# Performance work log

Measured on AMD Instinct MI355X. Metric: run time of the kernel, lower is better.

## Reference

```python
import jax, jax.numpy as jnp
import numpy as np

RADIUS = 3
T_STEPS = 2
NEG = -9.0e8
B, L, DEG = 256, 64, 6
FEAT, BOND, FP, OUT = 39, 10, 256, 1


def _leaky(x):
    return jax.nn.leaky_relu(x, 0.01)


def _gru(x, h, wih, whh, bih, bhh):
    # PyTorch GRUCell: gates ordered (r, z, n)
    gi = x @ wih.T + bih
    gh = h @ whh.T + bhh
    ir, iz, inn = jnp.split(gi, 3, axis=-1)
    hr, hz, hn = jnp.split(gh, 3, axis=-1)
    r = jax.nn.sigmoid(ir + hr)
    z = jax.nn.sigmoid(iz + hz)
    n = jnp.tanh(inn + r * hn)
    return (1.0 - z) * n + z * h


def _forward(atom_list, bond_list, atom_mask,
             atom_fc_w, atom_fc_b, neighbor_fc_w, neighbor_fc_b,
             align_w, align_b, attend_w, attend_b,
             gru_wih, gru_whh, gru_bih, gru_bhh,
             mol_align_w, mol_align_b, mol_attend_w, mol_attend_b,
             mol_gru_wih, mol_gru_whh, mol_gru_bih, mol_gru_bhh,
             out_w, out_b,
             atom_degree_list, bond_degree_list):
    b, l, _ = atom_list.shape
    mask = atom_mask[..., None]                                   # [B,L,1]
    atom_feature = _leaky(atom_list @ atom_fc_w.T + atom_fc_b)    # [B,L,FP]

    # per-molecule neighbor gather (padding index = L-1)
    bidx = jnp.arange(b)[:, None, None]
    atom_nb = atom_list[bidx, atom_degree_list]                    # [B,L,deg,FEAT]
    bond_nb = bond_list[bidx, bond_degree_list]                    # [B,L,deg,BOND]
    neighbor_feature = _leaky(
        jnp.concatenate([atom_nb, bond_nb], axis=-1) @ neighbor_fc_w.T + neighbor_fc_b
    )                                                              # [B,L,deg,FP]

    attend_mask = (atom_degree_list != l - 1).astype(atom_feature.dtype)[..., None]
    softmax_mask = jnp.where(atom_degree_list == l - 1, NEG, 0.0).astype(atom_feature.dtype)[..., None]

    for d in range(RADIUS):
        af_exp = jnp.broadcast_to(atom_feature[:, :, None, :], neighbor_feature.shape)
        feature_align = jnp.concatenate([af_exp, neighbor_feature], axis=-1)  # [B,L,deg,2FP]
        align_score = _leaky(feature_align @ align_w[d].T + align_b[d]) + softmax_mask
        attention_weight = jax.nn.softmax(align_score, axis=-2) * attend_mask
        attended = neighbor_feature @ attend_w[d].T + attend_b[d]
        context = jax.nn.elu(jnp.sum(attention_weight * attended, axis=-2))   # [B,L,FP]
        atom_feature = _gru(context.reshape(b * l, -1), atom_feature.reshape(b * l, -1),
                            gru_wih[d], gru_whh[d], gru_bih[d], gru_bhh[d]).reshape(b, l, -1)
        # faithful to original: self-feature broadcast across neighbor dim
        neighbor_feature = jnp.broadcast_to(jax.nn.relu(atom_feature)[:, :, None, :],
                                            neighbor_feature.shape)

    mol_feature = jnp.sum(jax.nn.relu(atom_feature) * mask, axis=-2)          # [B,FP]
    mol_softmax_mask = jnp.where(atom_mask == 0, NEG, 0.0).astype(atom_feature.dtype)[..., None]

    for _ in range(T_STEPS):
        m_exp = jnp.broadcast_to(mol_feature[:, None, :], atom_feature.shape)
        mol_align = jnp.concatenate([m_exp, atom_feature], axis=-1)           # [B,L,2FP]
        mol_score = _leaky(mol_align @ mol_align_w.T + mol_align_b) + mol_softmax_mask
        mol_w = jax.nn.softmax(mol_score, axis=-2) * mask
        attended = atom_feature @ mol_attend_w.T + mol_attend_b
        mol_context = jax.nn.elu(jnp.sum(mol_w * attended, axis=-2))
        mol_feature = _gru(mol_context, mol_feature,
                           mol_gru_wih, mol_gru_whh, mol_gru_bih, mol_gru_bhh)

    mol_prediction = mol_feature @ out_w.T + out_b
    return atom_feature, mol_prediction


def setup_inputs() -> dict:
    key = jax.random.key(0)
    ks = jax.random.split(key, 20)
    s = 0.05
    return {
        "atom_list": jax.random.normal(ks[0], (B, L, FEAT), jnp.float32),
        "bond_list": jax.random.normal(ks[1], (B, L, BOND), jnp.float32),
        "atom_degree_list": jax.random.randint(ks[2], (B, L, DEG), 0, L),
        "bond_degree_list": jax.random.randint(ks[3], (B, L, DEG), 0, L),
        "atom_mask": jnp.ones((B, L), jnp.float32),
        "atom_fc_w": jax.random.normal(ks[4], (FP, FEAT)) * s,
        "atom_fc_b": jnp.zeros((FP,)),
        "neighbor_fc_w": jax.random.normal(ks[5], (FP, FEAT + BOND)) * s,
        "neighbor_fc_b": jnp.zeros((FP,)),
        "align_w": jax.random.normal(ks[6], (RADIUS, 1, 2 * FP)) * s,
        "align_b": jnp.zeros((RADIUS, 1)),
        "attend_w": jax.random.normal(ks[7], (RADIUS, FP, FP)) * s,
        "attend_b": jnp.zeros((RADIUS, FP)),
        "gru_wih": jax.random.normal(ks[8], (RADIUS, 3 * FP, FP)) * s,
        "gru_whh": jax.random.normal(ks[9], (RADIUS, 3 * FP, FP)) * s,
        "gru_bih": jnp.zeros((RADIUS, 3 * FP)),
        "gru_bhh": jnp.zeros((RADIUS, 3 * FP)),
        "mol_align_w": jax.random.normal(ks[10], (1, 2 * FP)) * s,
        "mol_align_b": jnp.zeros((1,)),
        "mol_attend_w": jax.random.normal(ks[11], (FP, FP)) * s,
        "mol_attend_b": jnp.zeros((FP,)),
        "mol_gru_wih": jax.random.normal(ks[12], (3 * FP, FP)) * s,
        "mol_gru_whh": jax.random.normal(ks[13], (3 * FP, FP)) * s,
        "mol_gru_bih": jnp.zeros((3 * FP,)),
        "mol_gru_bhh": jnp.zeros((3 * FP,)),
        "out_w": jax.random.normal(ks[14], (OUT, FP)) * s,
        "out_b": jnp.zeros((OUT,)),
    }


def reference(atom_list, bond_list, atom_degree_list, bond_degree_list, atom_mask,
              atom_fc_w, atom_fc_b, neighbor_fc_w, neighbor_fc_b,
              align_w, align_b, attend_w, attend_b,
              gru_wih, gru_whh, gru_bih, gru_bhh,
              mol_align_w, mol_align_b, mol_attend_w, mol_attend_b,
              mol_gru_wih, mol_gru_whh, mol_gru_bih, mol_gru_bhh,
              out_w, out_b):
    return _forward(atom_list, bond_list, atom_mask,
                    atom_fc_w, atom_fc_b, neighbor_fc_w, neighbor_fc_b,
                    align_w, align_b, attend_w, attend_b,
                    gru_wih, gru_whh, gru_bih, gru_bhh,
                    mol_align_w, mol_align_b, mol_attend_w, mol_attend_b,
                    mol_gru_wih, mol_gru_whh, mol_gru_bih, mol_gru_bhh,
                    out_w, out_b,
                    atom_degree_list, bond_degree_list)
```

## Files before the change

kernel.cpp:

```cpp
#include <hip/hip_runtime.h>
#include <hip/hip_bf16.h>

#define NB 256
#define NL 64
#define DEG 6
#define FEAT 39
#define BOND 10
#define FP 256
#define NEGV (-9.0e8f)

using s16x8 = __attribute__((ext_vector_type(8))) short;
using f32x4 = __attribute__((ext_vector_type(4))) float;

__device__ __forceinline__ unsigned short f2bf(float f){
  unsigned u = __float_as_uint(f);
  u += 0x7fffu + ((u >> 16) & 1u);
  return (unsigned short)(u >> 16);
}
__device__ __forceinline__ float lo16(unsigned u){ return __uint_as_float(u << 16); }
__device__ __forceinline__ float hi16(unsigned u){ return __uint_as_float(u & 0xffff0000u); }

__device__ __forceinline__ float block_sum256(float v, float* scr){
  #pragma unroll
  for(int o=32;o>0;o>>=1) v += __shfl_down(v, o, 64);
  __syncthreads();
  if((threadIdx.x & 63) == 0) scr[threadIdx.x >> 6] = v;
  __syncthreads();
  return scr[0] + scr[1] + scr[2] + scr[3];
}
__device__ __forceinline__ float wave_allsum(float v){
  #pragma unroll
  for(int o=1;o<64;o<<=1) v += __shfl_xor(v, o, 64);
  return v;
}

#define CVT_N0 196608
#define CVT_N1 589824
#define CVT_N2 589824
#define CVT_N3 65536
#define CVT_N4 196608
#define CVT_N5 196608
#define CVT_TOT (CVT_N0+CVT_N1+CVT_N2+CVT_N3+CVT_N4+CVT_N5)

__global__ void k_cvt_all(const float* __restrict__ a0, const float* __restrict__ a1,
                          const float* __restrict__ a2, const float* __restrict__ a3,
                          const float* __restrict__ a4, const float* __restrict__ a5,
                          unsigned short* __restrict__ dst){
  int i = blockIdx.x*256 + threadIdx.x;
  int off = i; const float* src;
  if(off < CVT_N0) src = a0;
  else { off -= CVT_N0;
    if(off < CVT_N1) src = a1;
    else { off -= CVT_N1;
      if(off < CVT_N2) src = a2;
      else { off -= CVT_N2;
        if(off < CVT_N3) src = a3;
        else { off -= CVT_N3;
          if(off < CVT_N4) src = a4;
          else { off -= CVT_N4; src = a5; } } } } }
  dst[i] = f2bf(src[off]);
}

__global__ void k_tr(const float* __restrict__ aw, const float* __restrict__ nw,
                     float* __restrict__ afcT, unsigned short* __restrict__ nfcT){
  int i = blockIdx.x*256 + threadIdx.x;
  if(i < 40*256){
    int k = i >> 8, r = i & 255;
    afcT[i] = (k < FEAT) ? aw[r*FEAT + k] : 0.f;
  } else {
    int j = i - 40*256;
    int k = j >> 8, r = j & 255;
    nfcT[j] = (k < FEAT+BOND) ? f2bf(nw[r*(FEAT+BOND) + k]) : (unsigned short)0;
  }
}

__global__ __launch_bounds__(256) void k_atom4(const float* __restrict__ atom,
    const float* __restrict__ afcT, const float* __restrict__ bias, float* __restrict__ af){
  __shared__ float WT[40*256];
  __shared__ float x_s[4][40];
  const int t = threadIdx.x, bl0 = blockIdx.x*4;
  for(int v=t; v<2560; v+=256) *(float4*)&WT[v*4] = *(const float4*)&afcT[v*4];
  for(int idx=t; idx<4*FEAT; idx+=256){ int a=idx/FEAT, k=idx%FEAT; x_s[a][k]=atom[(bl0+a)*FEAT+k]; }
  if(t < 4) x_s[t][39] = 0.f;
  __syncthreads();
  const int w = t>>6, t0 = (t&63)*4, row = bl0 + w;
  float4 b4 = *(const float4*)&bias[t0];
  float acc[4] = {b4.x, b4.y, b4.z, b4.w};
  for(int k=0;k<40;++k){
    float iv = x_s[w][k];
    float4 wv = *(const float4*)&WT[(k<<8)+t0];
    acc[0]=fmaf(iv,wv.x,acc[0]); acc[1]=fmaf(iv,wv.y,acc[1]);
    acc[2]=fmaf(iv,wv.z,acc[2]); acc[3]=fmaf(iv,wv.w,acc[3]);
  }
  float4 o;
  o.x = acc[0]>0.f?acc[0]:0.01f*acc[0]; o.y = acc[1]>0.f?acc[1]:0.01f*acc[1];
  o.z = acc[2]>0.f?acc[2]:0.01f*acc[2]; o.w = acc[3]>0.f?acc[3]:0.01f*acc[3];
  *(float4*)&af[(size_t)row*FP + t0] = o;
}

__global__ __launch_bounds__(256) void k_nbr4(const float* __restrict__ atom,
    const float* __restrict__ bond, const int* __restrict__ adl, const int* __restrict__ bdl,
    const unsigned short* __restrict__ nfcT, const float* __restrict__ bn,
    const float* __restrict__ alw, const float* __restrict__ alb,
    const float* __restrict__ af, float* __restrict__ wnf, float* __restrict__ swb){
  __shared__ unsigned short WnT[52*256];
  __shared__ float in_s[4][DEG][52];
  __shared__ int   ai_s[4][DEG];
  const int t = threadIdx.x, bl0 = blockIdx.x*4;
  if(t < 24){ int a=t/6, d=t%6; ai_s[a][d] = adl[(bl0+a)*DEG + d]; }
  for(int v=t; v<1664; v+=256) *(s16x8*)&WnT[v*8] = *(const s16x8*)&nfcT[v*8];
  __syncthreads();
  for(int idx=t; idx<4*DEG*(FEAT+BOND); idx+=256){
    int a = idx/(DEG*(FEAT+BOND)), rem = idx%(DEG*(FEAT+BOND));
    int d = rem/(FEAT+BOND), k = rem%(FEAT+BOND);
    int bb = (bl0+a) >> 6;
    float v;
    if(k < FEAT) v = atom[((size_t)bb*NL + ai_s[a][d])*FEAT + k];
    else { int bi = bdl[(bl0+a)*DEG + d]; v = bond[((size_t)bb*NL + bi)*BOND + (k-FEAT)]; }
    in_s[a][d][k] = v;
  }
  if(t < 24){ int a=t/6, d=t%6; in_s[a][d][49]=0.f; in_s[a][d][50]=0.f; in_s[a][d][51]=0.f; }
  __syncthreads();
  const int w = t>>6, lane = t&63, t0 = lane*4, row = bl0 + w;
  float acc[DEG][4] = {};
  for(int k=0;k<52;++k){
    uint2 u = *(const uint2*)&WnT[(k<<8) + t0];
    float w0=lo16(u.x), w1=hi16(u.x), w2=lo16(u.y), w3=hi16(u.y);
    #pragma unroll
    for(int d=0;d<DEG;++d){
      float iv = in_s[w][d][k];
      acc[d][0]=fmaf(iv,w0,acc[d][0]); acc[d][1]=fmaf(iv,w1,acc[d][1]);
      acc[d][2]=fmaf(iv,w2,acc[d][2]); acc[d][3]=fmaf(iv,w3,acc[d][3]);
    }
  }
  float4 bnv = *(const float4*)&bn[t0];
  float bna[4] = {bnv.x, bnv.y, bnv.z, bnv.w};
  float nf[DEG][4];
  #pragma unroll
  for(int d=0;d<DEG;++d)
    #pragma unroll
    for(int j=0;j<4;++j){ float v = acc[d][j] + bna[j]; nf[d][j] = v>0.f ? v : 0.01f*v; }
  float4 af4 = *(const float4*)&af[(size_t)row*FP + t0];
  float4 a1  = *(const float4*)&alw[t0];
  float4 a2  = *(const float4*)&alw[FP + t0];
  float sa = wave_allsum(af4.x*a1.x + af4.y*a1.y + af4.z*a1.z + af4.w*a1.w);
  float sd[DEG];
  #pragma unroll
  for(int d=0;d<DEG;++d)
    sd[d] = wave_allsum(nf[d][0]*a2.x + nf[d][1]*a2.y + nf[d][2]*a2.z + nf[d][3]*a2.w);
  float ab = alb[0];
  float sc[DEG], msk[DEG];
  #pragma unroll
  for(int d=0;d<DEG;++d){
    float v = sa + sd[d] + ab;
    v = v>0.f ? v : 0.01f*v;
    msk[d] = (ai_s[w][d] == NL-1) ? 0.f : 1.f;
    sc[d] = v + (msk[d] > 0.f ? 0.f : NEGV);
  }
  float m = sc[0];
  #pragma unroll
  for(int d=1;d<DEG;++d) m = fmaxf(m, sc[d]);
  float e[DEG], Z = 0.f;
  #pragma unroll
  for(int d=0;d<DEG;++d){ e[d] = expf(sc[d]-m); Z += e[d]; }
  float wgt[DEG], sw = 0.f;
  #pragma unroll
  for(int d=0;d<DEG;++d){ wgt[d] = e[d]/Z*msk[d]; sw += wgt[d]; }
  float o[4] = {};
  #pragma unroll
  for(int d=0;d<DEG;++d)
    #pragma unroll
    for(int j=0;j<4;++j) o[j] = fmaf(wgt[d], nf[d][j], o[j]);
  float4 ov; ov.x=o[0]; ov.y=o[1]; ov.z=o[2]; ov.w=o[3];
  *(float4*)&wnf[(size_t)row*FP + t0] = ov;
  if(lane == 0) swb[row] = sw;
}

template<int MODE>
__global__ __launch_bounds__(256) void k_ctx_gemm(
    const float* __restrict__ Xsrc, const float* __restrict__ swb,
    const unsigned short* __restrict__ Wbf, const float* __restrict__ bat,
    unsigned short* __restrict__ ctxbf){
  __shared__ unsigned short A_lds[64][264];
  __shared__ unsigned short B_lds[64][264];
  const int t = threadIdx.x;
  const int m0 = (blockIdx.x >> 2) * 64, n0 = (blockIdx.x & 3) * 64;
  const int rb = t >> 4, cb = (t & 15) * 16;
  for(int i=0;i<4;++i){
    int row = i*16 + rb;
    const float* src = Xsrc + (size_t)(m0+row)*FP + cb;
    float mult = MODE ? swb[m0+row] : 1.f;
    unsigned short tmp[16];
    #pragma unroll
    for(int q=0;q<4;++q){
      float4 v = ((const float4*)src)[q];
      if(MODE){ v.x=fmaxf(v.x,0.f)*mult; v.y=fmaxf(v.y,0.f)*mult;
                v.z=fmaxf(v.z,0.f)*mult; v.w=fmaxf(v.w,0.f)*mult; }
      tmp[q*4+0]=f2bf(v.x); tmp[q*4+1]=f2bf(v.y); tmp[q*4+2]=f2bf(v.z); tmp[q*4+3]=f2bf(v.w);
    }
    *(s16x8*)&A_lds[row][cb]   = *(s16x8*)&tmp[0];
    *(s16x8*)&A_lds[row][cb+8] = *(s16x8*)&tmp[8];
    const unsigned short* wsrc = Wbf + (size_t)(n0+row)*FP + cb;
    *(s16x8*)&B_lds[row][cb]   = *(const s16x8*)&wsrc[0];
    *(s16x8*)&B_lds[row][cb+8] = *(const s16x8*)&wsrc[8];
  }
  __syncthreads();
  const int w = t>>6, lane = t&63, lr = lane&15, ks = lane>>4;
  const int wr = (w>>1)*32, wc = (w&1)*32;
  f32x4 acc[2][2] = {};
  #pragma unroll
  for(int kk=0;kk<8;++kk){
    int ko = kk*32 + ks*8;
    s16x8 a0 = *(const s16x8*)&A_lds[wr+lr][ko];
    s16x8 a1 = *(const s16x8*)&A_lds[wr+16+lr][ko];
    s16x8 b0 = *(const s16x8*)&B_lds[wc+lr][ko];
    s16x8 b1 = *(const s16x8*)&B_lds[wc+16+lr][ko];
    acc[0][0] = __builtin_amdgcn_mfma_f32_16x16x32_bf16(a0,b0,acc[0][0],0,0,0);
    acc[0][1] = __builtin_amdgcn_mfma_f32_16x16x32_bf16(a0,b1,acc[0][1],0,0,0);
    acc[1][0] = __builtin_amdgcn_mfma_f32_16x16x32_bf16(a1,b0,acc[1][0],0,0,0);
    acc[1][1] = __builtin_amdgcn_mfma_f32_16x16x32_bf16(a1,b1,acc[1][1],0,0,0);
  }
  #pragma unroll
  for(int fm=0;fm<2;++fm)
    #pragma unroll
    for(int fn=0;fn<2;++fn){
      int n = n0 + wc + fn*16 + lr;
      float batv = bat[n];
      #pragma unroll
      for(int j=0;j<4;++j){
        int m = m0 + wr + fm*16 + ks*4 + j;
        float v = acc[fm][fn][j] + swb[m]*batv;
        v = v > 0.f ? v : expm1f(v);
        ctxbf[(size_t)m*FP + n] = f2bf(v);
      }
    }
}

__global__ __launch_bounds__(256) void k_gates_gru(
    const unsigned short* __restrict__ ctxbf, const float* __restrict__ h_glob,
    const unsigned short* __restrict__ wihbf, const unsigned short* __restrict__ whhbf,
    const float* __restrict__ bih, const float* __restrict__ bhh,
    float* __restrict__ h_out){
  __shared__ unsigned short A_ctx[32][40];
  __shared__ unsigned short A_h[32][40];
  __shared__ unsigned short B_lds[6][64][40];
  const int t = threadIdx.x;
  const int m0 = (blockIdx.x >> 2) * 32, nc = (blockIdx.x & 3) * 64;
  const int w = t>>6, lane = t&63, lr = lane&15, ks = lane>>4;
  const int mh = (w>>1)*16, nh = (w&1)*32;
  f32x4 acc[6][2] = {};
  for(int kk=0;kk<8;++kk){
    const int k0 = kk*32;
    __syncthreads();
    {
      int row = t>>3, c4 = (t&7)*4;
      *(uint2*)&A_ctx[row][c4] = *(const uint2*)(ctxbf + (size_t)(m0+row)*FP + k0 + c4);
      float4 hv = *(const float4*)(h_glob + (size_t)(m0+row)*FP + k0 + c4);
      unsigned short ht[4] = {f2bf(hv.x), f2bf(hv.y), f2bf(hv.z), f2bf(hv.w)};
      *(uint2*)&A_h[row][c4] = *(uint2*)ht;
    }
    #pragma unroll
    for(int i=0;i<6;++i){
      int idx = i*256 + t;
      int s = idx >> 8, rem = idx & 255;
      int row = rem >> 2, c8 = (rem & 3)*8;
      const unsigned short* wsrc = (s < 3)
          ? wihbf + (size_t)(s*FP + nc + row)*FP + k0 + c8
          : whhbf + (size_t)((s-3)*FP + nc + row)*FP + k0 + c8;
      *(s16x8*)&B_lds[s][row][c8] = *(const s16x8*)wsrc;
    }
    __syncthreads();
    s16x8 ac = *(const s16x8*)&A_ctx[mh+lr][ks*8];
    s16x8 ah = *(const s16x8*)&A_h[mh+lr][ks*8];
    #pragma unroll
    for(int s=0;s<6;++s){
      s16x8 a = (s < 3) ? ac : ah;
      #pragma unroll
      for(int fn=0;fn<2;++fn){
        s16x8 b = *(const s16x8*)&B_lds[s][nh+fn*16+lr][ks*8];
        acc[s][fn] = __builtin_amdgcn_mfma_f32_16x16x32_bf16(a,b,acc[s][fn],0,0,0);
      }
    }
  }
  #pragma unroll
  for(int fn=0;fn<2;++fn){
    int n = nc + nh + fn*16 + lr;
    float bir = bih[n], biz = bih[FP+n], bin_ = bih[2*FP+n];
    float bhr = bhh[n], bhz = bhh[FP+n], bhn  = bhh[2*FP+n];
    #pragma unroll
    for(int j=0;j<4;++j){
      int m = m0 + mh + ks*4 + j;
      float h = h_glob[(size_t)m*FP + n];
      float ir = acc[0][fn][j]+bir, iz = acc[1][fn][j]+biz, inn = acc[2][fn][j]+bin_;
      float hr = acc[3][fn][j]+bhr, hz = acc[4][fn][j]+bhz, hn  = acc[5][fn][j]+bhn;
      float r = 1.f/(1.f + expf(-(ir+hr)));
      float z = 1.f/(1.f + expf(-(iz+hz)));
      float ng = tanhf(inn + r*hn);
      h_out[(size_t)m*FP + n] = (1.f-z)*ng + z*h;
    }
  }
}

__global__ __launch_bounds__(256) void k_lin_gemm(
    const float* __restrict__ Xsrc, const unsigned short* __restrict__ Wbf,
    const float* __restrict__ bias, float* __restrict__ Y){
  __shared__ unsigned short A_lds[64][264];
  __shared__ unsigned short B_lds[64][264];
  const int t = threadIdx.x;
  const int m0 = (blockIdx.x >> 2) * 64, n0 = (blockIdx.x & 3) * 64;
  const int rb = t >> 4, cb = (t & 15) * 16;
  for(int i=0;i<4;++i){
    int row = i*16 + rb;
    const float* src = Xsrc + (size_t)(m0+row)*FP + cb;
    unsigned short tmp[16];
    #pragma unroll
    for(int q=0;q<4;++q){
      float4 v = ((const float4*)src)[q];
      tmp[q*4+0]=f2bf(v.x); tmp[q*4+1]=f2bf(v.y); tmp[q*4+2]=f2bf(v.z); tmp[q*4+3]=f2bf(v.w);
    }
    *(s16x8*)&A_lds[row][cb]   = *(s16x8*)&tmp[0];
    *(s16x8*)&A_lds[row][cb+8] = *(s16x8*)&tmp[8];
    const unsigned short* wsrc = Wbf + (size_t)(n0+row)*FP + cb;
    *(s16x8*)&B_lds[row][cb]   = *(const s16x8*)&wsrc[0];
    *(s16x8*)&B_lds[row][cb+8] = *(const s16x8*)&wsrc[8];
  }
  __syncthreads();
  const int w = t>>6, lane = t&63, lr = lane&15, ks = lane>>4;
  const int wr = (w>>1)*32, wc = (w&1)*32;
  f32x4 acc[2][2] = {};
  #pragma unroll
  for(int kk=0;kk<8;++kk){
    int ko = kk*32 + ks*8;
    s16x8 a0 = *(const s16x8*)&A_lds[wr+lr][ko];
    s16x8 a1 = *(const s16x8*)&A_lds[wr+16+lr][ko];
    s16x8 b0 = *(const s16x8*)&B_lds[wc+lr][ko];
    s16x8 b1 = *(const s16x8*)&B_lds[wc+16+lr][ko];
    acc[0][0] = __builtin_amdgcn_mfma_f32_16x16x32_bf16(a0,b0,acc[0][0],0,0,0);
    acc[0][1] = __builtin_amdgcn_mfma_f32_16x16x32_bf16(a0,b1,acc[0][1],0,0,0);
    acc[1][0] = __builtin_amdgcn_mfma_f32_16x16x32_bf16(a1,b0,acc[1][0],0,0,0);
    acc[1][1] = __builtin_amdgcn_mfma_f32_16x16x32_bf16(a1,b1,acc[1][1],0,0,0);
  }
  #pragma unroll
  for(int fm=0;fm<2;++fm)
    #pragma unroll
    for(int fn=0;fn<2;++fn){
      int n = n0 + wc + fn*16 + lr;
      float bv = bias[n];
      #pragma unroll
      for(int j=0;j<4;++j){
        int m = m0 + wr + fm*16 + ks*4 + j;
        Y[(size_t)m*FP + n] = acc[fm][fn][j] + bv;
      }
    }
}

__global__ void k_finalize(const float* __restrict__ af, const float* __restrict__ mask,
                           float* __restrict__ molfeat, float* __restrict__ out_af){
  const int b = blockIdx.x, t = threadIdx.x;
  __shared__ float msk_s[NL];
  if(t < NL) msk_s[t] = mask[b*NL + t];
  __syncthreads();
  float mf = 0.f;
  for(int l=0;l<NL;++l){
    float v = af[(size_t)(b*NL + l)*FP + t];
    out_af[(size_t)(b*NL + l)*FP + t] = v;
    mf = fmaf(fmaxf(v,0.f), msk_s[l], mf);
  }
  molfeat[b*FP + t] = mf;
}

__global__ void k_mol_ctx(const float* __restrict__ af, const float* __restrict__ att,
    const float* __restrict__ mfin, const float* __restrict__ maw,
    const float* __restrict__ mabp, const float* __restrict__ mask,
    unsigned short* __restrict__ ctxb){
  const int b = blockIdx.x, t = threadIdx.x;
  __shared__ float mf_s[FP];
  __shared__ float sc_s[NL], aw_s[NL], scr[4];
  mf_s[t] = mfin[b*FP + t];
  __syncthreads();
  float sa = block_sum256(maw[t]*mf_s[t], scr);
  int l = t >> 2, q = t & 3;
  float p = 0.f;
  {
    const float* ar = af + (size_t)(b*NL + l)*FP + q*64;
    const float* w2 = maw + FP + q*64;
    for(int k=0;k<64;++k) p = fmaf(ar[k], w2[k], p);
  }
  p += __shfl_xor(p, 1, 64);
  p += __shfl_xor(p, 2, 64);
  if(q == 0){
    float mv = mask[b*NL + l];
    float v = sa + p + mabp[0];
    v = v > 0.f ? v : 0.01f*v;
    sc_s[l] = v + (mv == 0.f ? NEGV : 0.f);
  }
  __syncthreads();
  if(t < NL){
    float s = sc_s[t];
    float m = s;
    #pragma unroll
    for(int o=32;o>0;o>>=1) m = fmaxf(m, __shfl_xor(m, o, 64));
    float e = expf(s - m);
    float Z = e;
    #pragma unroll
    for(int o=32;o>0;o>>=1) Z += __shfl_xor(Z, o, 64);
    aw_s[t] = e / Z * mask[b*NL + t];
  }
  __syncthreads();
  float acc = 0.f;
  for(int l2=0;l2<NL;++l2) acc = fmaf(aw_s[l2], att[(size_t)(b*NL + l2)*FP + t], acc);
  float c = acc > 0.f ? acc : expm1f(acc);
  ctxb[b*FP + t] = f2bf(c);
}

__global__ void k_out(const float* __restrict__ molfeat, const float* __restrict__ ow,
                      const float* __restrict__ ob, float* __restrict__ outp){
  const int b = blockIdx.x, t = threadIdx.x;
  __shared__ float scr[4];
  float s = block_sum256(molfeat[b*FP + t]*ow[t], scr);
  if(t == 0) outp[b] = s + ob[0];
}

__global__ void k_atom_fc(const float* __restrict__ atom, const float* __restrict__ W,
                          const float* __restrict__ bias, float* __restrict__ af){
  const int row = blockIdx.x;
  const int t = threadIdx.x;
  __shared__ float x[FEAT];
  if(t < FEAT) x[t] = atom[row*FEAT + t];
  __syncthreads();
  float acc = bias[t];
  const float* wr = W + t*FEAT;
  #pragma unroll
  for(int k=0;k<FEAT;++k) acc = fmaf(x[k], wr[k], acc);
  af[row*FP + t] = acc > 0.f ? acc : 0.01f*acc;
}

__global__ void k_nbr_align(const float* __restrict__ atom, const float* __restrict__ bond,
    const int* __restrict__ adl, const int* __restrict__ bdl,
    const float* __restrict__ Wn, const float* __restrict__ bn,
    const float* __restrict__ alw, const float* __restrict__ alb,
    const float* __restrict__ af, float* __restrict__ wnf, float* __restrict__ swb){
  const int bl = blockIdx.x;
  const int b  = bl >> 6;
  const int t  = threadIdx.x;
  __shared__ float in_s[DEG][FEAT+BOND];
  __shared__ float nf_s[DEG][FP];
  __shared__ float af_s[FP];
  __shared__ int   ai[DEG];
  __shared__ float msk[DEG];
  __shared__ float sc[DEG];
  __shared__ float scr[4];
  if(t < DEG){ int a = adl[bl*DEG + t]; ai[t] = a; msk[t] = (a == NL-1) ? 0.f : 1.f; }
  af_s[t] = af[bl*FP + t];
  __syncthreads();
  for(int idx = t; idx < DEG*(FEAT+BOND); idx += FP){
    int d = idx / (FEAT+BOND), k = idx % (FEAT+BOND);
    float v;
    if(k < FEAT) v = atom[(b*NL + ai[d])*FEAT + k];
    else { int bi = bdl[bl*DEG + d]; v = bond[(b*NL + bi)*BOND + (k-FEAT)]; }
    in_s[d][k] = v;
  }
  __syncthreads();
  float acc[DEG];
  #pragma unroll
  for(int d=0;d<DEG;++d) acc[d] = 0.f;
  const float* wr = Wn + t*(FEAT+BOND);
  for(int k=0;k<FEAT+BOND;++k){
    float w = wr[k];
    #pragma unroll
// ... 201 lines not shown
    float v = sa + p + mabp[0];
    v = v > 0.f ? v : 0.01f*v;
    sc_s[l] = v + (mv == 0.f ? NEGV : 0.f);
  }
  __syncthreads();
  if(t < NL){
    float s = sc_s[t];
    float m = s;
    #pragma unroll
    for(int o=32;o>0;o>>=1) m = fmaxf(m, __shfl_xor(m, o, 64));
    float e = expf(s - m);
    float Z = e;
    #pragma unroll
    for(int o=32;o>0;o>>=1) Z += __shfl_xor(Z, o, 64);
    aw_s[t] = e / Z * mask[b*NL + t];
  }
  __syncthreads();
  float acc = 0.f;
  for(int l2=0;l2<NL;++l2) acc = fmaf(aw_s[l2], att[(size_t)(b*NL + l2)*FP + t], acc);
  ctx_s[t] = acc > 0.f ? acc : expm1f(acc);
  __syncthreads();
  float air=0.f, aiz=0.f, ain=0.f, ahr=0.f, ahz=0.f, ahn=0.f;
  const float4* wirp=(const float4*)(wih + (size_t)t*FP);
  const float4* wizp=(const float4*)(wih + (size_t)(FP+t)*FP);
  const float4* winp=(const float4*)(wih + (size_t)(2*FP+t)*FP);
  const float4* whrp=(const float4*)(whh + (size_t)t*FP);
  const float4* whzp=(const float4*)(whh + (size_t)(FP+t)*FP);
  const float4* whnp=(const float4*)(whh + (size_t)(2*FP+t)*FP);
  for(int k4=0;k4<FP/4;++k4){
    float4 xv = ((const float4*)ctx_s)[k4];
    float4 hv = ((const float4*)mf_s)[k4];
    float4 f0=wirp[k4], f1=wizp[k4], f2=winp[k4];
    float4 g0=whrp[k4], g1=whzp[k4], g2=whnp[k4];
    air=fmaf(xv.x,f0.x,air); air=fmaf(xv.y,f0.y,air); air=fmaf(xv.z,f0.z,air); air=fmaf(xv.w,f0.w,air);
    aiz=fmaf(xv.x,f1.x,aiz); aiz=fmaf(xv.y,f1.y,aiz); aiz=fmaf(xv.z,f1.z,aiz); aiz=fmaf(xv.w,f1.w,aiz);
    ain=fmaf(xv.x,f2.x,ain); ain=fmaf(xv.y,f2.y,ain); ain=fmaf(xv.z,f2.z,ain); ain=fmaf(xv.w,f2.w,ain);
    ahr=fmaf(hv.x,g0.x,ahr); ahr=fmaf(hv.y,g0.y,ahr); ahr=fmaf(hv.z,g0.z,ahr); ahr=fmaf(hv.w,g0.w,ahr);
    ahz=fmaf(hv.x,g1.x,ahz); ahz=fmaf(hv.y,g1.y,ahz); ahz=fmaf(hv.z,g1.z,ahz); ahz=fmaf(hv.w,g1.w,ahz);
    ahn=fmaf(hv.x,g2.x,ahn); ahn=fmaf(hv.y,g2.y,ahn); ahn=fmaf(hv.z,g2.z,ahn); ahn=fmaf(hv.w,g2.w,ahn);
  }
  float ir=air+bih[t], iz=aiz+bih[FP+t], inn=ain+bih[2*FP+t];
  float hr=ahr+bhh[t], hz=ahz+bhh[FP+t], hn=ahn+bhh[2*FP+t];
  float rg = 1.f/(1.f + expf(-(ir+hr)));
  float zg = 1.f/(1.f + expf(-(iz+hz)));
  float ng = tanhf(inn + rg*hn);
  molfeat[b*FP + t] = (1.f-zg)*ng + zg*mf_s[t];
}

extern "C" void kernel_launch(void* const* d_in, const int* in_sizes, int n_in,
                              void* d_out, int out_size, void* d_ws, size_t ws_size,
                              hipStream_t stream){
  const float* atom_list = (const float*)d_in[0];
  const float* bond_list = (const float*)d_in[1];
  const int*   adl       = (const int*)d_in[2];
  const int*   bdl       = (const int*)d_in[3];
  const float* amask     = (const float*)d_in[4];
  const float* afc_w     = (const float*)d_in[5];
  const float* afc_b     = (const float*)d_in[6];
  const float* nfc_w     = (const float*)d_in[7];
  const float* nfc_b     = (const float*)d_in[8];
  const float* align_w   = (const float*)d_in[9];
  const float* align_b   = (const float*)d_in[10];
  const float* attend_w  = (const float*)d_in[11];
  const float* attend_b  = (const float*)d_in[12];
  const float* gru_wih   = (const float*)d_in[13];
  const float* gru_whh   = (const float*)d_in[14];
  const float* gru_bih   = (const float*)d_in[15];
  const float* gru_bhh   = (const float*)d_in[16];
  const float* mol_align_w  = (const float*)d_in[17];
  const float* mol_align_b  = (const float*)d_in[18];
  const float* mol_attend_w = (const float*)d_in[19];
  const float* mol_attend_b = (const float*)d_in[20];
  const float* mg_wih    = (const float*)d_in[21];
  const float* mg_whh    = (const float*)d_in[22];
  const float* mg_bih    = (const float*)d_in[23];
  const float* mg_bhh    = (const float*)d_in[24];
  const float* out_w     = (const float*)d_in[25];
  const float* out_b     = (const float*)d_in[26];

  float* out_af   = (float*)d_out;
  float* out_pred = out_af + (size_t)NB*NL*FP;

  const size_t NROW = (size_t)NB*NL;
  const size_t F32_CNT = 3*NROW*FP + NROW + 2*(size_t)NB*FP + 40*256;
  const size_t BF16_CNT = NROW*FP + CVT_TOT + 52*256;
  const size_t NEED = F32_CNT*4 + BF16_CNT*2;

  if(ws_size >= NEED){
    float* af_a    = (float*)d_ws;
    float* af_b    = af_a + NROW*FP;
    float* wnf     = af_b + NROW*FP;
    float* swb     = wnf  + NROW*FP;
    float* mf_a    = swb  + NROW;
    float* mf_b    = mf_a + (size_t)NB*FP;
    float* afcT    = mf_b + (size_t)NB*FP;
    unsigned short* ctxbf   = (unsigned short*)(afcT + 40*256);
    unsigned short* attw_bf = ctxbf + NROW*FP;
    unsigned short* wih_bf  = attw_bf + CVT_N0;
    unsigned short* whh_bf  = wih_bf + CVT_N1;
    unsigned short* maw_bf  = whh_bf + CVT_N2;
    unsigned short* mgih_bf = maw_bf + CVT_N3;
    unsigned short* mghh_bf = mgih_bf + CVT_N4;
    unsigned short* nfcT_bf = mghh_bf + CVT_N5;

    k_cvt_all<<<CVT_TOT/256, 256, 0, stream>>>(attend_w, gru_wih, gru_whh,
                                               mol_attend_w, mg_wih, mg_whh, attw_bf);
    k_tr<<<(40*256 + 52*256)/256, 256, 0, stream>>>(afc_w, nfc_w, afcT, nfcT_bf);

    k_atom4<<<NB*NL/4, 256, 0, stream>>>(atom_list, afcT, afc_b, af_a);
    k_nbr4<<<NB*NL/4, 256, 0, stream>>>(atom_list, bond_list, adl, bdl,
                                        nfcT_bf, nfc_b, align_w, align_b, af_a, wnf, swb);
    float* h_cur = af_a;
    float* h_nxt = af_b;
    for(int d=0; d<3; ++d){
      const unsigned short* Wat = attw_bf + (size_t)d*FP*FP;
      const float* bat = attend_b + (size_t)d*FP;
      const unsigned short* wih = wih_bf + (size_t)d*3*FP*FP;
      const unsigned short* whh = whh_bf + (size_t)d*3*FP*FP;
      const float* bih = gru_bih + (size_t)d*3*FP;
      const float* bhh = gru_bhh + (size_t)d*3*FP;
      if(d == 0)
        k_ctx_gemm<0><<<(NB*NL/64)*4, 256, 0, stream>>>(wnf, swb, Wat, bat, ctxbf);
      else
        k_ctx_gemm<1><<<(NB*NL/64)*4, 256, 0, stream>>>(h_cur, swb, Wat, bat, ctxbf);
      k_gates_gru<<<(NB*NL/32)*4, 256, 0, stream>>>(ctxbf, h_cur, wih, whh, bih, bhh, h_nxt);
      float* tmp = h_cur; h_cur = h_nxt; h_nxt = tmp;
    }
    k_lin_gemm<<<(NB*NL/64)*4, 256, 0, stream>>>(h_cur, maw_bf, mol_attend_b, wnf);
    k_finalize<<<NB, 256, 0, stream>>>(h_cur, amask, mf_a, out_af);
    float* m_cur = mf_a; float* m_nxt = mf_b;
    for(int s=0; s<2; ++s){
      k_mol_ctx<<<NB, 256, 0, stream>>>(h_cur, wnf, m_cur, mol_align_w, mol_align_b,
                                        amask, ctxbf);
      k_gates_gru<<<(NB/32)*4, 256, 0, stream>>>(ctxbf, m_cur, mgih_bf, mghh_bf,
                                                 mg_bih, mg_bhh, m_nxt);
      float* tmp = m_cur; m_cur = m_nxt; m_nxt = tmp;
    }
    k_out<<<NB, 256, 0, stream>>>(m_cur, out_w, out_b, out_pred);
  } else {
    float* af      = (float*)d_ws;
    float* wnf     = af  + NROW*FP;
    float* swb     = wnf + NROW*FP;
    float* molfeat = swb + NROW;

    k_atom_fc<<<NB*NL, FP, 0, stream>>>(atom_list, afc_w, afc_b, af);
    k_nbr_align<<<NB*NL, FP, 0, stream>>>(atom_list, bond_list, adl, bdl,
                                          nfc_w, nfc_b, align_w, align_b, af, wnf, swb);
    for(int d=0; d<3; ++d){
      const float* Wat = attend_w + (size_t)d*FP*FP;
      const float* bat = attend_b + (size_t)d*FP;
      const float* wih = gru_wih + (size_t)d*3*FP*FP;
      const float* whh = gru_whh + (size_t)d*3*FP*FP;
      const float* bih = gru_bih + (size_t)d*3*FP;
      const float* bhh = gru_bhh + (size_t)d*3*FP;
      if(d == 0) k_ctx_gru<0><<<NB*NL/16, FP, 0, stream>>>(wnf, swb, af, Wat, bat, wih, whh, bih, bhh);
      else       k_ctx_gru<1><<<NB*NL/16, FP, 0, stream>>>(af,  swb, af, Wat, bat, wih, whh, bih, bhh);
    }
    k_mol_att<<<NB, FP, 0, stream>>>(af, mol_attend_w, mol_attend_b, amask, wnf, molfeat, out_af);
    for(int s=0; s<2; ++s)
      k_mol_step<<<NB, FP, 0, stream>>>(af, wnf, molfeat, mol_align_w, mol_align_b, amask,
                                        mg_wih, mg_whh, mg_bih, mg_bhh);
    k_out<<<NB, FP, 0, stream>>>(molfeat, out_w, out_b, out_pred);
  }
}
```

Baseline: 337.6 us.

## Fuse all three radius iterations into one persistent MFMA kernel with packed weights

Replaces the per-radius context GEMM and GRU gates kernels (six launches) with a single kernel, k_radius2. Each 64-row block keeps its context tile in LDS and runs all three radius steps in place. The attend and GRU weights are repacked on the device into an MFMA fragment order and double-buffered through LDS with register prefetch. This removes the global round trips for the bf16 context and the second hidden-state buffer. The trade-offs are 256 blocks of 512 threads, which may underfill the GPU, and a larger LDS footprint per block. The diff also vectorizes a dot product in the molecule context kernel with float4 loads.

```diff
diff --git a/kernel.cpp b/kernel.cpp
--- a/kernel.cpp
+++ b/kernel.cpp
@@ -34,31 +34,58 @@
   return v;
 }
 
-#define CVT_N0 196608
-#define CVT_N1 589824
-#define CVT_N2 589824
-#define CVT_N3 65536
-#define CVT_N4 196608
-#define CVT_N5 196608
-#define CVT_TOT (CVT_N0+CVT_N1+CVT_N2+CVT_N3+CVT_N4+CVT_N5)
-
-__global__ void k_cvt_all(const float* __restrict__ a0, const float* __restrict__ a1,
-                          const float* __restrict__ a2, const float* __restrict__ a3,
-                          const float* __restrict__ a4, const float* __restrict__ a5,
-                          unsigned short* __restrict__ dst){
+#define MCVT_N0 65536
+#define MCVT_N1 196608
+#define MCVT_N2 196608
+#define MCVT_TOT (MCVT_N0+MCVT_N1+MCVT_N2)
+#define CTXPK_N (3*8*8192)
+#define GPK_N   (3*2*8*24576)
+#define HALF_U16 24576
+
+__global__ void k_cvt_mol(const float* __restrict__ a0, const float* __restrict__ a1,
+                          const float* __restrict__ a2, unsigned short* __restrict__ dst){
   int i = blockIdx.x*256 + threadIdx.x;
+  if(i >= MCVT_TOT) return;
   int off = i; const float* src;
-  if(off < CVT_N0) src = a0;
-  else { off -= CVT_N0;
-    if(off < CVT_N1) src = a1;
-    else { off -= CVT_N1;
-      if(off < CVT_N2) src = a2;
-      else { off -= CVT_N2;
-        if(off < CVT_N3) src = a3;
-        else { off -= CVT_N3;
-          if(off < CVT_N4) src = a4;
-          else { off -= CVT_N4; src = a5; } } } } }
+  if(off < MCVT_N0) src = a0;
+  else { off -= MCVT_N0;
+    if(off < MCVT_N1) src = a1;
+    else { off -= MCVT_N1; src = a2; } }
   dst[i] = f2bf(src[off]);
+}
+
+__global__ void k_pack(const float* __restrict__ attend_w, const float* __restrict__ gru_wih,
+                       const float* __restrict__ gru_whh,
+                       unsigned short* __restrict__ ctx_pk, unsigned short* __restrict__ gates_pk){
+  int i = blockIdx.x*256 + threadIdx.x;
+  if(i < CTXPK_N){
+    int d = i >> 16;
+    int rem = i & 65535;
+    int kk = rem >> 13;
+    int r2 = rem & 8191;
+    int g = r2 >> 9;
+    int l = (r2 >> 3) & 63;
+    int q = r2 & 7;
+    int row = g*16 + (l & 15);
+    int k = kk*32 + (l >> 4)*8 + q;
+    ctx_pk[i] = f2bf(attend_w[((size_t)d*256 + row)*256 + k]);
+  } else {
+    int j = i - CTXPK_N;
+    if(j >= GPK_N) return;
+    int d = j / 393216;
+    int rem = j - d*393216;
+    int nc = rem / 196608; rem -= nc*196608;
+    int kk = rem / 24576;  rem -= kk*24576;
+    int f = rem >> 9;
+    int l = (rem >> 3) & 63;
+    int q = rem & 7;
+    int s = f >> 3, g = f & 7;
+    int row = nc*128 + g*16 + (l & 15);
+    int k = kk*32 + (l >> 4)*8 + q;
+    float v = (s < 3) ? gru_wih[(((size_t)d*3 + s)*256 + row)*256 + k]
+                      : gru_whh[(((size_t)d*3 + (s-3))*256 + row)*256 + k];
+    gates_pk[j] = f2bf(v);
+  }
 }
 
 __global__ void k_tr(const float* __restrict__ aw, const float* __restrict__ nw,
@@ -176,11 +203,202 @@
   if(lane == 0) swb[row] = sw;
 }
 
-template<int MODE>
-__global__ __launch_bounds__(256) void k_ctx_gemm(
-    const float* __restrict__ Xsrc, const float* __restrict__ swb,
-    const unsigned short* __restrict__ Wbf, const float* __restrict__ bat,
-    unsigned short* __restrict__ ctxbf){
+__global__ __launch_bounds__(512) void k_radius2(
+    const float* __restrict__ wnf, float* __restrict__ af, const float* __restrict__ swb,
+    const unsigned short* __restrict__ ctx_pk, const unsigned short* __restrict__ gates_pk,
+    const float* __restrict__ attend_b,
+    const float* __restrict__ gru_bih, const float* __restrict__ gru_bhh){
+  __shared__ __align__(16) unsigned short Cf[32*512];
+  __shared__ __align__(16) unsigned short Bu[2][HALF_U16];
+  const int t = threadIdx.x;
+  const int w = t>>6, lane = t&63, lr = lane&15, ks = lane>>4;
+  const int wm = w>>2, wn = w&3;
+  const int m0 = blockIdx.x*64;
+
+  s16x8 pf[6]; int pfn = 2;
+  auto LOADT = [&](const unsigned short* src, int n){
+    pfn = n;
+    #pragma unroll
+    for(int c=0;c<6;++c) if(c < n) pf[c] = *(const s16x8*)(src + (w + c*8)*512 + lane*8);
+  };
+  auto WRITET = [&](int h){
+    #pragma unroll
+    for(int c=0;c<6;++c) if(c < pfn) *(s16x8*)&Bu[h][(w + c*8)*512 + lane*8] = pf[c];
+  };
+
+  LOADT(ctx_pk, 2);
+  WRITET(0);
+  int half = 0;
+
+  for(int d=0; d<3; ++d){
+    const float* bat  = attend_b + d*256;
+    const float* bihd = gru_bih + d*768;
+    const float* bhhd = gru_bhh + d*768;
+    f32x4 acc2[2][4] = {};
+    for(int kk=0; kk<8; ++kk){
+      __syncthreads();
+      if(kk < 7) LOADT(ctx_pk + ((size_t)d*8 + kk+1)*8192, 2);
+      else       LOADT(gates_pk + ((size_t)(d*2 + 0)*8 + 0)*24576, 6);
+      s16x8 xf[2];
+      #pragma unroll
+      for(int mf=0; mf<2; ++mf){
+        int row = m0 + wm*32 + mf*16 + lr;
+        float4 v0, v1;
+        if(d == 0){
+          const float* sp = wnf + (size_t)row*256 + kk*32 + ks*8;
+          v0 = *(const float4*)sp; v1 = *(const float4*)(sp+4);
+        } else {
+          const float* sp = af + (size_t)row*256 + kk*32 + ks*8;
+          v0 = *(const float4*)sp; v1 = *(const float4*)(sp+4);
+          float sw = swb[row];
+          v0.x=fmaxf(v0.x,0.f)*sw; v0.y=fmaxf(v0.y,0.f)*sw;
+          v0.z=fmaxf(v0.z,0.f)*sw; v0.w=fmaxf(v0.w,0.f)*sw;
+          v1.x=fmaxf(v1.x,0.f)*sw; v1.y=fmaxf(v1.y,0.f)*sw;
+          v1.z=fmaxf(v1.z,0.f)*sw; v1.w=fmaxf(v1.w,0.f)*sw;
+        }
+        unsigned short tmp[8] = {f2bf(v0.x),f2bf(v0.y),f2bf(v0.z),f2bf(v0.w),
+                                 f2bf(v1.x),f2bf(v1.y),f2bf(v1.z),f2bf(v1.w)};
+        xf[mf] = *(s16x8*)tmp;
+      }
+      #pragma unroll
+      for(int nf=0; nf<4; ++nf){
+        s16x8 wf = *(const s16x8*)&Bu[half][((wn*4 + nf)*64 + lane)*8];
+        acc2[0][nf] = __builtin_amdgcn_mfma_f32_16x16x32_bf16(wf, xf[0], acc2[0][nf],0,0,0);
+        acc2[1][nf] = __builtin_amdgcn_mfma_f32_16x16x32_bf16(wf, xf[1], acc2[1][nf],0,0,0);
+      }
+      WRITET(half^1);
+      half ^= 1;
+    }
+    #pragma unroll
+    for(int mf=0; mf<2; ++mf){
+      float swv = swb[m0 + wm*32 + mf*16 + lr];
+      #pragma unroll
+      for(int nf=0; nf<4; ++nf){
+        int nb = wn*64 + nf*16 + ks*4;
+        float4 b4 = *(const float4*)&bat[nb];
+        float bj[4] = {b4.x, b4.y, b4.z, b4.w};
+        unsigned short o4[4];
+        #pragma unroll
+        for(int j=0;j<4;++j){
+          float v = acc2[mf][nf][j] + swv*bj[j];
+          v = v > 0.f ? v : expm1f(v);
+          o4[j] = f2bf(v);
+        }
+        int gm = wm*2 + mf;
+        int kkp = wn*2 + (nf>>1);
+        int lhi = ((nf & 1) << 1) | (ks >> 1);
+        int addr = (gm*8 + kkp)*512 + (lhi*16 + lr)*8 + (ks & 1)*4;
+        *(uint2*)&Cf[addr] = *(uint2*)o4;
+      }
+    }
+    float hnew0[2][2][4];
+    for(int nc=0; nc<2; ++nc){
+      f32x4 aR[2][2] = {}, aZ[2][2] = {}, aN[2][2] = {}, aH[2][2] = {};
+      for(int kk=0; kk<8; ++kk){
+        __syncthreads();
+        bool last = (nc == 1) && (kk == 7);
+        if(!last){
+          if(kk < 7)      LOADT(gates_pk + ((size_t)(d*2 + nc)*8 + kk+1)*24576, 6);
+          else            LOADT(gates_pk + ((size_t)(d*2 + 1)*8 + 0)*24576, 6);
+        } else if(d < 2){
+          LOADT(ctx_pk + ((size_t)(d+1)*8 + 0)*8192, 2);
+        }
+        s16x8 hf[2];
+        #pragma unroll
+        for(int mf=0; mf<2; ++mf){
+          int row = m0 + wm*32 + mf*16 + lr;
+          const float* sp = af + (size_t)row*256 + kk*32 + ks*8;
+          float4 v0 = *(const float4*)sp, v1 = *(const float4*)(sp+4);
+          unsigned short tmp[8] = {f2bf(v0.x),f2bf(v0.y),f2bf(v0.z),f2bf(v0.w),
+                                   f2bf(v1.x),f2bf(v1.y),f2bf(v1.z),f2bf(v1.w)};
+          hf[mf] = *(s16x8*)tmp;
+        }
+        s16x8 cf0 = *(const s16x8*)&Cf[((wm*2 + 0)*8 + kk)*512 + lane*8];
+        s16x8 cf1 = *(const s16x8*)&Cf[((wm*2 + 1)*8 + kk)*512 + lane*8];
+        #pragma unroll
+        for(int fn=0; fn<2; ++fn){
+          int g = wn*2 + fn;
+          s16x8 b0 = *(const s16x8*)&Bu[half][((0*8 + g)*64 + lane)*8];
+          s16x8 b1 = *(const s16x8*)&Bu[half][((1*8 + g)*64 + lane)*8];
+          s16x8 b2 = *(const s16x8*)&Bu[half][((2*8 + g)*64 + lane)*8];
+          s16x8 b3 = *(const s16x8*)&Bu[half][((3*8 + g)*64 + lane)*8];
+          s16x8 b4 = *(const s16x8*)&Bu[half][((4*8 + g)*64 + lane)*8];
+          s16x8 b5 = *(const s16x8*)&Bu[half][((5*8 + g)*64 + lane)*8];
+          aR[0][fn] = __builtin_amdgcn_mfma_f32_16x16x32_bf16(cf0, b0, aR[0][fn],0,0,0);
+          aR[1][fn] = __builtin_amdgcn_mfma_f32_16x16x32_bf16(cf1, b0, aR[1][fn],0,0,0);
+          aZ[0][fn] = __builtin_amdgcn_mfma_f32_16x16x32_bf16(cf0, b1, aZ[0][fn],0,0,0);
+          aZ[1][fn] = __builtin_amdgcn_mfma_f32_16x16x32_bf16(cf1, b1, aZ[1][fn],0,0,0);
+          aN[0][fn] = __builtin_amdgcn_mfma_f32_16x16x32_bf16(cf0, b2, aN[0][fn],0,0,0);
+          aN[1][fn] = __builtin_amdgcn_mfma_f32_16x16x32_bf16(cf1, b2, aN[1][fn],0,0,0);
+          aR[0][fn] = __builtin_amdgcn_mfma_f32_16x16x32_bf16(hf[0], b3, aR[0][fn],0,0,0);
+          aR[1][fn] = __builtin_amdgcn_mfma_f32_16x16x32_bf16(hf[1], b3, aR[1][fn],0,0,0);
+          aZ[0][fn] = __builtin_amdgcn_mfma_f32_16x16x32_bf16(hf[0], b4, aZ[0][fn],0,0,0);
+          aZ[1][fn] = __builtin_amdgcn_mfma_f32_16x16x32_bf16(hf[1], b4, aZ[1][fn],0,0,0);
+          aH[0][fn] = __builtin_amdgcn_mfma_f32_16x16x32_bf16(hf[0], b5, aH[0][fn],0,0,0);
+          aH[1][fn] = __builtin_amdgcn_mfma_f32_16x16x32_bf16(hf[1], b5, aH[1][fn],0,0,0);
+        }
+        if(!last || d < 2) WRITET(half^1);
+        half ^= 1;
+      }
+      if(nc == 0){
+        #pragma unroll
+        for(int mf=0; mf<2; ++mf)
+          #pragma unroll
+          for(int fn=0; fn<2; ++fn){
+            int n = wn*32 + fn*16 + lr;
+            float brz = bihd[n] + bhhd[n];
+            float bzz = bihd[256+n] + bhhd[256+n];
+            float bnn = bihd[512+n];
+            float bhn = bhhd[512+n];
+            #pragma unroll
+            for(int j=0;j<4;++j){
+              int m = m0 + wm*32 + mf*16 + ks*4 + j;
+              float hold = af[(size_t)m*256 + n];
+              float r = 1.f/(1.f + expf(-(aR[mf][fn][j] + brz)));
+              float z = 1.f/(1.f + expf(-(aZ[mf][fn][j] + bzz)));
+              float ng = tanhf(aN[mf][fn][j] + bnn + r*(aH[mf][fn][j] + bhn));
+              hnew0[mf][fn][j] = (1.f - z)*ng + z*hold;
+            }
+          }
+      } else {
+        #pragma unroll
+        for(int mf=0; mf<2; ++mf)
+          #pragma unroll
+          for(int fn=0; fn<2; ++fn){
+            int n = 128 + wn*32 + fn*16 + lr;
+            float brz = bihd[n] + bhhd[n];
+            float bzz = bihd[256+n] + bhhd[256+n];
+            float bnn = bihd[512+n];
+            float bhn = bhhd[512+n];
+            #pragma unroll
+            for(int j=0;j<4;++j){
+              int m = m0 + wm*32 + mf*16 + ks*4 + j;
+              float hold = af[(size_t)m*256 + n];
+              float r = 1.f/(1.f + expf(-(aR[mf][fn][j] + brz)));
+              float z = 1.f/(1.f + expf(-(aZ[mf][fn][j] + bzz)));
+              float ng = tanhf(aN[mf][fn][j] + bnn + r*(aH[mf][fn][j] + bhn));
+              af[(size_t)m*256 + n] = (1.f - z)*ng + z*hold;
+            }
+          }
+        #pragma unroll
+        for(int mf=0; mf<2; ++mf)
+          #pragma unroll
+          for(int fn=0; fn<2; ++fn){
+            int n = wn*32 + fn*16 + lr;
+            #pragma unroll
+            for(int j=0;j<4;++j){
+              int m = m0 + wm*32 + mf*16 + ks*4 + j;
+              af[(size_t)m*256 + n] = hnew0[mf][fn][j];
+            }
+          }
+      }
+    }
+  }
+}
+
+__global__ __launch_bounds__(256) void k_lin_gemm(
+    const float* __restrict__ Xsrc, const unsigned short* __restrict__ Wbf,
+    const float* __restrict__ bias, float* __restrict__ Y){
   __shared__ unsigned short A_lds[64][264];
   __shared__ unsigned short B_lds[64][264];
   const int t = threadIdx.x;
@@ -189,13 +407,10 @@
   for(int i=0;i<4;++i){
     int row = i*16 + rb;
     const float* src = Xsrc + (size_t)(m0+row)*FP + cb;
-    float mult = MODE ? swb[m0+row] : 1.f;
     unsigned short tmp[16];
     #pragma unroll
     for(int q=0;q<4;++q){
       float4 v = ((const float4*)src)[q];
-      if(MODE){ v.x=fmaxf(v.x,0.f)*mult; v.y=fmaxf(v.y,0.f)*mult;
-                v.z=fmaxf(v.z,0.f)*mult; v.w=fmaxf(v.w,0.f)*mult; }
       tmp[q*4+0]=f2bf(v.x); tmp[q*4+1]=f2bf(v.y); tmp[q*4+2]=f2bf(v.z); tmp[q*4+3]=f2bf(v.w);
     }
     *(s16x8*)&A_lds[row][cb]   = *(s16x8*)&tmp[0];
@@ -225,18 +440,16 @@
     #pragma unroll
     for(int fn=0;fn<2;++fn){
       int n = n0 + wc + fn*16 + lr;
-      float batv = bat[n];
+      float bv = bias[n];
       #pragma unroll
       for(int j=0;j<4;++j){
         int m = m0 + wr + fm*16 + ks*4 + j;
-        float v = acc[fm][fn][j] + swb[m]*batv;
-        v = v > 0.f ? v : expm1f(v);
-        ctxbf[(size_t)m*FP + n] = f2bf(v);
+        Y[(size_t)m*FP + n] = acc[fm][fn][j] + bv;
       }
     }
 }
 
-__global__ __launch_bounds__(256) void k_gates_gru(
+__global__ __launch_bounds__(256) void k_gates32(
     const unsigned short* __restrict__ ctxbf, const float* __restrict__ h_glob,
     const unsigned short* __restrict__ wihbf, const unsigned short* __restrict__ whhbf,
     const float* __restrict__ bih, const float* __restrict__ bhh,
@@ -301,59 +514,6 @@
   }
 }
 
-__global__ __launch_bounds__(256) void k_lin_gemm(
-    const float* __restrict__ Xsrc, const unsigned short* __restrict__ Wbf,
-    const float* __restrict__ bias, float* __restrict__ Y){
-  __shared__ unsigned short A_lds[64][264];
-  __shared__ unsigned short B_lds[64][264];
-  const int t = threadIdx.x;
-  const int m0 = (blockIdx.x >> 2) * 64, n0 = (blockIdx.x & 3) * 64;
-  const int rb = t >> 4, cb = (t & 15) * 16;
-  for(int i=0;i<4;++i){
-    int row = i*16 + rb;
-    const float* src = Xsrc + (size_t)(m0+row)*FP + cb;
-    unsigned short tmp[16];
-    #pragma unroll
-    for(int q=0;q<4;++q){
-      float4 v = ((const float4*)src)[q];
-      tmp[q*4+0]=f2bf(v.x); tmp[q*4+1]=f2bf(v.y); tmp[q*4+2]=f2bf(v.z); tmp[q*4+3]=f2bf(v.w);
-    }
-    *(s16x8*)&A_lds[row][cb]   = *(s16x8*)&tmp[0];
-    *(s16x8*)&A_lds[row][cb+8] = *(s16x8*)&tmp[8];
-    const unsigned short* wsrc = Wbf + (size_t)(n0+row)*FP + cb;
-    *(s16x8*)&B_lds[row][cb]   = *(const s16x8*)&wsrc[0];
-    *(s16x8*)&B_lds[row][cb+8] = *(const s16x8*)&wsrc[8];
-  }
-  __syncthreads();
-  const int w = t>>6, lane = t&63, lr = lane&15, ks = lane>>4;
-  const int wr = (w>>1)*32, wc = (w&1)*32;
-  f32x4 acc[2][2] = {};
-  #pragma unroll
-  for(int kk=0;kk<8;++kk){
-    int ko = kk*32 + ks*8;
-    s16x8 a0 = *(const s16x8*)&A_lds[wr+lr][ko];
-    s16x8 a1 = *(const s16x8*)&A_lds[wr+16+lr][ko];
-    s16x8 b0 = *(const s16x8*)&B_lds[wc+lr][ko];
-    s16x8 b1 = *(const s16x8*)&B_lds[wc+16+lr][ko];
-    acc[0][0] = __builtin_amdgcn_mfma_f32_16x16x32_bf16(a0,b0,acc[0][0],0,0,0);
-    acc[0][1] = __builtin_amdgcn_mfma_f32_16x16x32_bf16(a0,b1,acc[0][1],0,0,0);
-    acc[1][0] = __builtin_amdgcn_mfma_f32_16x16x32_bf16(a1,b0,acc[1][0],0,0,0);
-    acc[1][1] = __builtin_amdgcn_mfma_f32_16x16x32_bf16(a1,b1,acc[1][1],0,0,0);
-  }
-  #pragma unroll
-  for(int fm=0;fm<2;++fm)
-    #pragma unroll
-    for(int fn=0;fn<2;++fn){
-      int n = n0 + wc + fn*16 + lr;
-      float bv = bias[n];
-      #pragma unroll
-      for(int j=0;j<4;++j){
-        int m = m0 + wr + fm*16 + ks*4 + j;
-        Y[(size_t)m*FP + n] = acc[fm][fn][j] + bv;
-      }
-    }
-}
-
 __global__ void k_finalize(const float* __restrict__ af, const float* __restrict__ mask,
                            float* __restrict__ molfeat, float* __restrict__ out_af){
   const int b = blockIdx.x, t = threadIdx.x;
@@ -382,9 +542,14 @@
   int l = t >> 2, q = t & 3;
   float p = 0.f;
   {
-    const float* ar = af + (size_t)(b*NL + l)*FP + q*64;
-    const float* w2 = maw + FP + q*64;
-    for(int k=0;k<64;++k) p = fmaf(ar[k], w2[k], p);
+    const float4* ar = (const float4*)(af + (size_t)(b*NL + l)*FP + q*64);
+    const float4* w2 = (const float4*)(maw + FP + q*64);
+    #pragma unroll
+    for(int k=0;k<16;++k){
+      float4 a = ar[k], ww = w2[k];
+      p = fmaf(a.x,ww.x,p); p = fmaf(a.y,ww.y,p);
+      p = fmaf(a.z,ww.z,p); p = fmaf(a.w,ww.w,p);
+    }
   }
   p += __shfl_xor(p, 1, 64);
   p += __shfl_xor(p, 2, 64);
@@ -752,58 +917,42 @@
   float* out_pred = out_af + (size_t)NB*NL*FP;
 
   const size_t NROW = (size_t)NB*NL;
-  const size_t F32_CNT = 3*NROW*FP + NROW + 2*(size_t)NB*FP + 40*256;
-  const size_t BF16_CNT = NROW*FP + CVT_TOT + 52*256;
-  const size_t NEED = F32_CNT*4 + BF16_CNT*2;
+  const size_t F32_CNT = 2*NROW*FP + NROW + 2*(size_t)NB*FP + 40*256;
+  const size_t U16_CNT = (size_t)NB*FP + MCVT_TOT + 52*256 + CTXPK_N + GPK_N;
+  const size_t NEED = F32_CNT*4 + U16_CNT*2;
 
   if(ws_size >= NEED){
     float* af_a    = (float*)d_ws;
-    float* af_b    = af_a + NROW*FP;
-    float* wnf     = af_b + NROW*FP;
+    float* wnf     = af_a + NROW*FP;
     float* swb     = wnf  + NROW*FP;
     float* mf_a    = swb  + NROW;
     float* mf_b    = mf_a + (size_t)NB*FP;
     float* afcT    = mf_b + (size_t)NB*FP;
-    unsigned short* ctxbf   = (unsigned short*)(afcT + 40*256);
-    unsigned short* attw_bf = ctxbf + NROW*FP;
-    unsigned short* wih_bf  = attw_bf + CVT_N0;
-    unsigned short* whh_bf  = wih_bf + CVT_N1;
-    unsigned short* maw_bf  = whh_bf + CVT_N2;
-    unsigned short* mgih_bf = maw_bf + CVT_N3;
-    unsigned short* mghh_bf = mgih_bf + CVT_N4;
-    unsigned short* nfcT_bf = mghh_bf + CVT_N5;
-
-    k_cvt_all<<<CVT_TOT/256, 256, 0, stream>>>(attend_w, gru_wih, gru_whh,
-                                               mol_attend_w, mg_wih, mg_whh, attw_bf);
+    unsigned short* ctxbf_m = (unsigned short*)(afcT + 40*256);
+    unsigned short* maw_bf  = ctxbf_m + (size_t)NB*FP;
+    unsigned short* mgih_bf = maw_bf + MCVT_N0;
+    unsigned short* mghh_bf = mgih_bf + MCVT_N1;
+    unsigned short* nfcT_bf = mghh_bf + MCVT_N2;
+    unsigned short* ctx_pk  = nfcT_bf + 52*256;
+    unsigned short* gates_pk= ctx_pk + CTXPK_N;
+
+    k_cvt_mol<<<(MCVT_TOT+255)/256, 256, 0, stream>>>(mol_attend_w, mg_wih, mg_whh, maw_bf);
+    k_pack<<<(CTXPK_N+GPK_N)/256, 256, 0, stream>>>(attend_w, gru_wih, gru_whh, ctx_pk, gates_pk);
     k_tr<<<(40*256 + 52*256)/256, 256, 0, stream>>>(afc_w, nfc_w, afcT, nfcT_bf);
 
     k_atom4<<<NB*NL/4, 256, 0, stream>>>(atom_list, afcT, afc_b, af_a);
     k_nbr4<<<NB*NL/4, 256, 0, stream>>>(atom_list, bond_list, adl, bdl,
                                         nfcT_bf, nfc_b, align_w, align_b, af_a, wnf, swb);
-    float* h_cur = af_a;
-    float* h_nxt = af_b;
-    for(int d=0; d<3; ++d){
-      const unsigned short* Wat = attw_bf + (size_t)d*FP*FP;
-      const float* bat = attend_b + (size_t)d*FP;
-      const unsigned short* wih = wih_bf + (size_t)d*3*FP*FP;
-      const unsigned short* whh = whh_bf + (size_t)d*3*FP*FP;
-      const float* bih = gru_bih + (size_t)d*3*FP;
-      const float* bhh = gru_bhh + (size_t)d*3*FP;
-      if(d == 0)
-        k_ctx_gemm<0><<<(NB*NL/64)*4, 256, 0, stream>>>(wnf, swb, Wat, bat, ctxbf);
-      else
-        k_ctx_gemm<1><<<(NB*NL/64)*4, 256, 0, stream>>>(h_cur, swb, Wat, bat, ctxbf);
-      k_gates_gru<<<(NB*NL/32)*4, 256, 0, stream>>>(ctxbf, h_cur, wih, whh, bih, bhh, h_nxt);
-      float* tmp = h_cur; h_cur = h_nxt; h_nxt = tmp;
-    }
-    k_lin_gemm<<<(NB*NL/64)*4, 256, 0, stream>>>(h_cur, maw_bf, mol_attend_b, wnf);
-    k_finalize<<<NB, 256, 0, stream>>>(h_cur, amask, mf_a, out_af);
+    k_radius2<<<NB*NL/64, 512, 0, stream>>>(wnf, af_a, swb, ctx_pk, gates_pk,
+                                            attend_b, gru_bih, gru_bhh);
+    k_lin_gemm<<<(NB*NL/64)*4, 256, 0, stream>>>(af_a, maw_bf, mol_attend_b, wnf);
+    k_finalize<<<NB, 256, 0, stream>>>(af_a, amask, mf_a, out_af);
     float* m_cur = mf_a; float* m_nxt = mf_b;
     for(int s=0; s<2; ++s){
-      k_mol_ctx<<<NB, 256, 0, stream>>>(h_cur, wnf, m_cur, mol_align_w, mol_align_b,
-                                        amask, ctxbf);
-      k_gates_gru<<<(NB/32)*4, 256, 0, stream>>>(ctxbf, m_cur, mgih_bf, mghh_bf,
-                                                 mg_bih, mg_bhh, m_nxt);
+      k_mol_ctx<<<NB, 256, 0, stream>>>(af_a, wnf, m_cur, mol_align_w, mol_align_b,
+                                        amask, ctxbf_m);
+      k_gates32<<<(NB/32)*4, 256, 0, stream>>>(ctxbf_m, m_cur, mgih_bf, mghh_bf,
+                                               mg_bih, mg_bhh, m_nxt);
       float* tmp = m_cur; m_cur = m_nxt; m_nxt = tmp;
     }
     k_out<<<NB, 256, 0, stream>>>(m_cur, out_w, out_b, out_pred);
```

After: 323.6 us. 4.2% less time.
